# Performance work log

Hardware: AMD Instinct MI355X
Metric: run time of the kernel (lower is better)

## Reference

```python
import jax, jax.numpy as jnp
import numpy as np


def setup_inputs() -> dict:
    key = jax.random.key(0)
    ks = jax.random.split(key, 8)
    b, s1, s2 = 16, 512, 40
    video_dim, text_dim, attn_dim = 1024, 300, 256
    return {
        "video": jax.random.normal(ks[0], (b, s1, video_dim), dtype=jnp.float32),
        "text": jax.random.normal(ks[1], (b, s2, text_dim), dtype=jnp.float32),
        "w1": jax.random.normal(ks[2], (video_dim, attn_dim), dtype=jnp.float32),
        "w2": jax.random.normal(ks[3], (text_dim, attn_dim), dtype=jnp.float32),
        "w3": jax.random.normal(ks[4], (attn_dim, 1), dtype=jnp.float32),
        "bias": jax.random.normal(ks[5], (attn_dim,), dtype=jnp.float32),
        "w4": jax.random.normal(ks[6], (4 * attn_dim, 500), dtype=jnp.float32),
        "b4": jax.random.normal(ks[7], (500,), dtype=jnp.float32),
    }


def reference(video, text, w1, w2, w3, bias, w4, b4):
    # video: (b, s1, d1), text: (b, s2, d2)
    e = jnp.einsum("bsd,da->bsa", video, w1)   # (b, s1, a) -- also 'hh' in original
    f = jnp.einsum("btd,da->bta", text, w2)    # (b, s2, a)
    # additive attention energies: tanh over (b, s1, s2, a) broadcast sum
    h = jnp.tanh(e[:, :, None, :] + f[:, None, :, :] + bias)  # (b, s1, s2, a)
    logits = jnp.squeeze(jnp.einsum("bsta,ao->bsto", h, w3), -1)  # (b, s1, s2)
    # original expands logits over attn_dim then softmaxes dim=2; identical to
    # softmax over s2 of the scalar scores, broadcast afterwards.
    attn = jax.nn.softmax(logits, axis=2)  # (b, s1, s2)
    text_attn = jnp.einsum("bst,bta->bsa", attn, f)  # (b, s1, a)
    cont = jnp.concatenate(
        [e, text_attn, e * text_attn, e - text_attn], axis=-1
    )  # (b, s1, 4a)
    return jnp.tanh(cont) @ w4 + b4  # (b, s1, 500)
```

## Files before the change

kernel.cpp:

```cpp
#include <hip/hip_runtime.h>
#include <hip/hip_bf16.h>
#include <cstdint>

typedef __attribute__((ext_vector_type(8))) short bf16x8;
typedef __attribute__((ext_vector_type(4))) short bf16x4;
typedef __attribute__((ext_vector_type(4))) float f32x4;

#define TANH_SCALE 2.8853900817779268f
#define TANH_UNSCALE 0.34657359027997264f

__device__ __forceinline__ short cvt_bf16(float f) {
  union { float f; uint32_t u; } x; x.f = f;
  uint32_t r = x.u + 0x7FFFu + ((x.u >> 16) & 1u);
  return (short)(r >> 16);
}
__device__ __forceinline__ float bf16_to_f(short s) {
  union { uint32_t u; float f; } x; x.u = ((uint32_t)(uint16_t)s) << 16;
  return x.f;
}

__device__ __forceinline__ float tanh_fast(float x) {
  float e = __builtin_amdgcn_exp2f(x * TANH_SCALE);
  return 1.0f - 2.0f * __builtin_amdgcn_rcpf(e + 1.0f);
}
__device__ __forceinline__ float sig_pre(float xs) {
  float e = __builtin_amdgcn_exp2f(xs);
  return __builtin_amdgcn_rcpf(e + 1.0f);
}

__device__ __forceinline__ void split8(float4 a, float4 b, bf16x8& h, bf16x8& l) {
  float fa[8] = {a.x, a.y, a.z, a.w, b.x, b.y, b.z, b.w};
  uint32_t uh[8], ul[8];
  #pragma unroll
  for (int j = 0; j < 8; j++) {
    union { float f; uint32_t u; } x; x.f = fa[j];
    uh[j] = x.u;
    union { uint32_t u; float f; } t; t.u = x.u & 0xffff0000u;
    union { float f; uint32_t u; } y; y.f = fa[j] - t.f;
    ul[j] = y.u;
  }
  union { uint32_t w[4]; bf16x8 v; } H, L;
  #pragma unroll
  for (int j = 0; j < 4; j++) {
    H.w[j] = __builtin_amdgcn_perm(uh[2 * j + 1], uh[2 * j], 0x07060302u);
    L.w[j] = __builtin_amdgcn_perm(ul[2 * j + 1], ul[2 * j], 0x07060302u);
  }
  h = H.v; l = L.v;
}

__global__ __launch_bounds__(256) void k_prep(const float* __restrict__ text,
                                              const float* __restrict__ w1,
                                              const float* __restrict__ w2,
                                              const float* __restrict__ w4,
                                              short* __restrict__ w1h,
                                              short* __restrict__ w1l,
                                              short* __restrict__ w4T,
                                              short* __restrict__ th,
                                              short* __restrict__ tl,
                                              short* __restrict__ w2h,
                                              short* __restrict__ w2l) {
  __shared__ float tile[32][33];
  int bid = blockIdx.x;
  if (bid < 256) {
    int idx = bid;
    int r0 = (idx & 31) * 32, c0 = (idx >> 5) * 32;
    int j = threadIdx.x & 31, i0 = threadIdx.x >> 5;
    #pragma unroll
    for (int i = i0; i < 32; i += 8) tile[i][j] = w1[(size_t)(r0 + i) * 256 + c0 + j];
    __syncthreads();
    #pragma unroll
    for (int i = i0; i < 32; i += 8) {
      float v = tile[j][i];
      short h = cvt_bf16(v);
      w1h[(size_t)(c0 + i) * 1024 + r0 + j] = h;
      w1l[(size_t)(c0 + i) * 1024 + r0 + j] = cvt_bf16(v - bf16_to_f(h));
    }
  } else if (bid < 768) {
    int idx = bid - 256;
    int r0 = (idx & 31) * 32, c0 = (idx >> 5) * 32;
    int j = threadIdx.x & 31, i0 = threadIdx.x >> 5;
    #pragma unroll
    for (int i = i0; i < 32; i += 8) {
      int c = c0 + j;
      tile[i][j] = (c < 500) ? w4[(size_t)(r0 + i) * 500 + c] : 0.f;
    }
    __syncthreads();
    #pragma unroll
    for (int i = i0; i < 32; i += 8)
      w4T[(size_t)(c0 + i) * 1024 + r0 + j] = cvt_bf16(tile[j][i]);
  } else if (bid < 928) {
    int idx = bid - 768;
    int row = idx * 4 + (threadIdx.x >> 6);
    int cl = threadIdx.x & 63;
    const float* trow = text + (size_t)row * 300;
    short* hrow = th + (size_t)row * 320;
    short* lrow = tl + (size_t)row * 320;
    #pragma unroll
    for (int c0 = 0; c0 < 320; c0 += 64) {
      int c = c0 + cl;
      float v = (c < 300) ? trow[c] : 0.f;
      short h = cvt_bf16(v);
      hrow[c] = h;
      lrow[c] = cvt_bf16(v - bf16_to_f(h));
    }
  } else {
    int idx = bid - 928;
    int rt = idx % 10, ct = idx / 10;
    int r0 = rt * 32, c0 = ct * 32;
    int j = threadIdx.x & 31, i0 = threadIdx.x >> 5;
    #pragma unroll
    for (int i = i0; i < 32; i += 8) {
      int r = r0 + i;
      tile[i][j] = (r < 300) ? w2[(size_t)r * 256 + c0 + j] : 0.f;
    }
    __syncthreads();
    #pragma unroll
    for (int i = i0; i < 32; i += 8) {
      float v = tile[j][i];
      short h = cvt_bf16(v);
      w2h[(size_t)(c0 + i) * 320 + r0 + j] = h;
      w2l[(size_t)(c0 + i) * 320 + r0 + j] = cvt_bf16(v - bf16_to_f(h));
    }
  }
}

__device__ __forceinline__ void load_lds16(void* lds, const void* g) {
  __builtin_amdgcn_global_load_lds(
      (const __attribute__((address_space(1))) void*)g,
      (__attribute__((address_space(3))) void*)lds, 16, 0, 0);
}

__global__ __launch_bounds__(256) void k_gemm_big(const float* __restrict__ video,
                                                  const short* __restrict__ w1h,
                                                  const short* __restrict__ w1l,
                                                  const short* __restrict__ th,
                                                  const short* __restrict__ tl,
                                                  const short* __restrict__ w2h,
                                                  const short* __restrict__ w2l,
                                                  float* __restrict__ eparts,
                                                  float* __restrict__ fbuf) {
  __shared__ __align__(16) char smem[65536];
  int bid = blockIdx.x;
  int tid = threadIdx.x, lane = tid & 63, wave = tid >> 6;
  int mrow = lane & 15, quad = lane >> 4;

  if (bid < 512) {
    short (*Ash)[64] = (short (*)[64])(smem);
    short (*Asl)[64] = (short (*)[64])(smem + 16384);
    int m0 = (bid & 63) * 128, n0 = ((bid >> 6) & 3) * 64;
    int z = bid >> 8;
    int kz0 = z * 512;
    int wm = wave * 32;
    int lrow = lane >> 3, lseg = (lane & 7) * 8;

    f32x4 acc[2][4];
    #pragma unroll
    for (int i = 0; i < 2; i++)
      #pragma unroll
      for (int j = 0; j < 4; j++) acc[i][j] = (f32x4){0.f, 0.f, 0.f, 0.f};

    auto stageB = [&](int k0, int buf) {
      short* Bh = (short*)(smem + 32768 + buf * 8192);
      short* Bl = (short*)(smem + 49152 + buf * 8192);
      #pragma unroll
      for (int i = 0; i < 2; i++) {
        int c = wave * 2 + i;
        size_t go = (size_t)(n0 + c * 8 + lrow) * 1024 + k0 + lseg;
        load_lds16(Bh + (size_t)(c * 8) * 64, w1h + go);
        load_lds16(Bl + (size_t)(c * 8) * 64, w1l + go);
      }
    };
    auto loadA = [&](int k0, float4* va) {
      #pragma unroll
      for (int it = 0; it < 4; it++) {
        int idx = it * 256 + tid;
        const float* src = video + (size_t)(m0 + (idx >> 3)) * 1024 + k0 + (idx & 7) * 8;
        va[it * 2]     = *(const float4*)src;
        va[it * 2 + 1] = *(const float4*)(src + 4);
      }
    };

    float4 va[8];
    stageB(kz0, 0);
    loadA(kz0, va);

    for (int t = 0; t < 8; t++) {
      int k0 = kz0 + t * 64;
      int cur = t & 1;
      bf16x8 hi[4], lo[4];
      #pragma unroll
      for (int it = 0; it < 4; it++) split8(va[it * 2], va[it * 2 + 1], hi[it], lo[it]);
      __builtin_amdgcn_s_barrier();
      #pragma unroll
      for (int it = 0; it < 4; it++) {
        int idx = it * 256 + tid;
        *(bf16x8*)&Ash[idx >> 3][(idx & 7) * 8] = hi[it];
        *(bf16x8*)&Asl[idx >> 3][(idx & 7) * 8] = lo[it];
      }
      if (t + 1 < 8) {
        stageB(k0 + 64, cur ^ 1);
        loadA(k0 + 64, va);
        asm volatile("s_waitcnt vmcnt(12)" ::: "memory");
      } else {
        asm volatile("s_waitcnt vmcnt(0)" ::: "memory");
      }
      asm volatile("s_waitcnt lgkmcnt(0)" ::: "memory");
      __builtin_amdgcn_s_barrier();
      const short* Bh = (const short*)(smem + 32768 + cur * 8192);
      const short* Bl = (const short*)(smem + 49152 + cur * 8192);
      #pragma unroll
      for (int ks = 0; ks < 2; ks++) {
        int kk = ks * 32 + quad * 8;
        bf16x8 ah[2], al[2], bh[4], bl[4];
        #pragma unroll
        for (int i = 0; i < 2; i++) {
          ah[i] = *(const bf16x8*)&Ash[wm + i * 16 + mrow][kk];
          al[i] = *(const bf16x8*)&Asl[wm + i * 16 + mrow][kk];
        }
        #pragma unroll
        for (int j = 0; j < 4; j++) {
          bh[j] = *(const bf16x8*)&Bh[(size_t)(j * 16 + mrow) * 64 + kk];
          bl[j] = *(const bf16x8*)&Bl[(size_t)(j * 16 + mrow) * 64 + kk];
        }
        #pragma unroll
        for (int i = 0; i < 2; i++)
          #pragma unroll
          for (int j = 0; j < 4; j++) {
            acc[i][j] = __builtin_amdgcn_mfma_f32_16x16x32_bf16(ah[i], bh[j], acc[i][j], 0, 0, 0);
            acc[i][j] = __builtin_amdgcn_mfma_f32_16x16x32_bf16(ah[i], bl[j], acc[i][j], 0, 0, 0);
            acc[i][j] = __builtin_amdgcn_mfma_f32_16x16x32_bf16(al[i], bh[j], acc[i][j], 0, 0, 0);
          }
      }
    }
    float* C = eparts + (size_t)z * 8192 * 256;
    int rbase = quad * 4;
    #pragma unroll
    for (int i = 0; i < 2; i++)
      #pragma unroll
      for (int j = 0; j < 4; j++) {
        int col = n0 + j * 16 + mrow;
        #pragma unroll
        for (int r = 0; r < 4; r++) {
          int row = m0 + wm + i * 16 + rbase + r;
          C[(size_t)row * 256 + col] = acc[i][j][r];
        }
      }
  } else {
    short (*Ash)[72] = (short (*)[72])(smem);
    short (*Asl)[72] = (short (*)[72])(smem + 9216);
    short (*Bsh)[72] = (short (*)[72])(smem + 18432);
    short (*Bsl)[72] = (short (*)[72])(smem + 27648);
    int idx = bid - 512;
    int m0 = (idx % 10) * 64, n0 = (idx / 10) * 64;
    int wm = (wave & 1) * 32, wn = (wave >> 1) * 32;
    int srow = tid >> 3, sseg = (tid & 7) * 8;
    f32x4 acc[2][2];
    #pragma unroll
    for (int i = 0; i < 2; i++)
      #pragma unroll
      for (int j = 0; j < 2; j++) acc[i][j] = (f32x4){0.f, 0.f, 0.f, 0.f};

    for (int k0 = 0; k0 < 320; k0 += 64) {
      size_t aoff0 = (size_t)(m0 + srow) * 320 + k0 + sseg;
      size_t aoff1 = aoff0 + (size_t)32 * 320;
      size_t boff0 = (size_t)(n0 + srow) * 320 + k0 + sseg;
      size_t boff1 = boff0 + (size_t)32 * 320;
      bf16x8 a0h = *(const bf16x8*)(th + aoff0);
      bf16x8 a1h = *(const bf16x8*)(th + aoff1);
      bf16x8 a0l = *(const bf16x8*)(tl + aoff0);
      bf16x8 a1l = *(const bf16x8*)(tl + aoff1);
      bf16x8 b0h = *(const bf16x8*)(w2h + boff0);
      bf16x8 b1h = *(const bf16x8*)(w2h + boff1);
      bf16x8 b0l = *(const bf16x8*)(w2l + boff0);
      bf16x8 b1l = *(const bf16x8*)(w2l + boff1);
      __syncthreads();
      *(bf16x8*)&Ash[srow][sseg] = a0h;  *(bf16x8*)&Ash[srow + 32][sseg] = a1h;
      *(bf16x8*)&Asl[srow][sseg] = a0l;  *(bf16x8*)&Asl[srow + 32][sseg] = a1l;
      *(bf16x8*)&Bsh[srow][sseg] = b0h;  *(bf16x8*)&Bsh[srow + 32][sseg] = b1h;
      *(bf16x8*)&Bsl[srow][sseg] = b0l;  *(bf16x8*)&Bsl[srow + 32][sseg] = b1l;
      __syncthreads();
      #pragma unroll
      for (int ks = 0; ks < 2; ks++) {
        int kk = ks * 32 + quad * 8;
        bf16x8 ah[2], al[2], bh[2], bl[2];
        ah[0] = *(const bf16x8*)&Ash[wm + mrow][kk];
        ah[1] = *(const bf16x8*)&Ash[wm + 16 + mrow][kk];
        al[0] = *(const bf16x8*)&Asl[wm + mrow][kk];
        al[1] = *(const bf16x8*)&Asl[wm + 16 + mrow][kk];
        bh[0] = *(const bf16x8*)&Bsh[wn + mrow][kk];
        bh[1] = *(const bf16x8*)&Bsh[wn + 16 + mrow][kk];
        bl[0] = *(const bf16x8*)&Bsl[wn + mrow][kk];
        bl[1] = *(const bf16x8*)&Bsl[wn + 16 + mrow][kk];
        #pragma unroll
        for (int i = 0; i < 2; i++)
          #pragma unroll
          for (int j = 0; j < 2; j++) {
            acc[i][j] = __builtin_amdgcn_mfma_f32_16x16x32_bf16(ah[i], bh[j], acc[i][j], 0, 0, 0);
            acc[i][j] = __builtin_amdgcn_mfma_f32_16x16x32_bf16(ah[i], bl[j], acc[i][j], 0, 0, 0);
            acc[i][j] = __builtin_amdgcn_mfma_f32_16x16x32_bf16(al[i], bh[j], acc[i][j], 0, 0, 0);
          }
      }
    }
    int rbase = quad * 4;
    #pragma unroll
    for (int i = 0; i < 2; i++)
      #pragma unroll
      for (int j = 0; j < 2; j++) {
        int col = n0 + wn + j * 16 + mrow;
        #pragma unroll
        for (int r = 0; r < 4; r++) {
          int row = m0 + wm + i * 16 + rbase + r;
          fbuf[(size_t)row * 256 + col] = acc[i][j][r];
        }
      }
  }
}

__global__ __launch_bounds__(256) void k_gemm_f(const short* __restrict__ A,
                                                const short* __restrict__ BT,
                                                const float* __restrict__ bias,
                                                float* __restrict__ C,
                                                int K, int ldc, int nstore) {
  __shared__ __align__(16) short As[2][128][64];
  __shared__ __align__(16) short Bs[2][64][64];
  int m0 = blockIdx.x * 128, n0 = blockIdx.y * 64;
  int tid = threadIdx.x, lane = tid & 63, wave = tid >> 6;
  int wm = wave * 32;
  int mrow = lane & 15, quad = lane >> 4;
  int lrow = lane >> 3, lseg = (lane & 7) * 8;

  f32x4 acc[2][4];
  #pragma unroll
  for (int i = 0; i < 2; i++)
    #pragma unroll
    for (int j = 0; j < 4; j++) acc[i][j] = (f32x4){0.f, 0.f, 0.f, 0.f};

  auto stage = [&](int k0, int buf) {
    #pragma unroll
    for (int i = 0; i < 4; i++) {
      int c = wave * 4 + i;
      load_lds16(&As[buf][c * 8][0], A + (size_t)(m0 + c * 8 + lrow) * K + k0 + lseg);
    }
    #pragma unroll
    for (int i = 0; i < 2; i++) {
      int c = wave * 2 + i;
      load_lds16(&Bs[buf][c * 8][0], BT + (size_t)(n0 + c * 8 + lrow) * K + k0 + lseg);
    }
  };

  int NT = K >> 6;
  stage(0, 0);
  for (int t = 0; t < NT; t++) {
    int cur = t & 1;
    if (t + 1 < NT) {
      stage((t + 1) << 6, cur ^ 1);
      asm volatile("s_waitcnt vmcnt(6)" ::: "memory");
    } else {
      asm volatile("s_waitcnt vmcnt(0)" ::: "memory");
    }
    __builtin_amdgcn_s_barrier();
    #pragma unroll
    for (int ks = 0; ks < 2; ks++) {
      int kk = ks * 32 + quad * 8;
      bf16x8 af[2], bf[4];
      #pragma unroll
      for (int i = 0; i < 2; i++) af[i] = *(const bf16x8*)&As[cur][wm + i * 16 + mrow][kk];
      #pragma unroll
      for (int j = 0; j < 4; j++) bf[j] = *(const bf16x8*)&Bs[cur][j * 16 + mrow][kk];
      #pragma unroll
      for (int i = 0; i < 2; i++)
        #pragma unroll
        for (int j = 0; j < 4; j++)
          acc[i][j] = __builtin_amdgcn_mfma_f32_16x16x32_bf16(af[i], bf[j], acc[i][j], 0, 0, 0);
    }
    __builtin_amdgcn_s_barrier();
  }
  int rbase = quad * 4;
  #pragma unroll
  for (int i = 0; i < 2; i++)
    #pragma unroll
    for (int j = 0; j < 4; j++) {
      int col = n0 + j * 16 + mrow;
      if (col < nstore) {
        float bv = bias[col];
        #pragma unroll
        for (int r = 0; r < 4; r++) {
          int row = m0 + wm + i * 16 + rbase + r;
          C[(size_t)row * ldc + col] = acc[i][j][r] + bv;
        }
      }
    }
}

__global__ __launch_bounds__(512) void k_middle(const float* __restrict__ e0p,
                                                const float* __restrict__ e1p,
                                                const float* __restrict__ fb,
                                                const float* __restrict__ w3,
                                                const float* __restrict__ bias,
                                                short* __restrict__ cont) {
  __shared__ __align__(16) float fbs[40 * 256];
  __shared__ float lg[16][40];
  __shared__ float attn[16][40];
  int tid = threadIdx.x, wave = tid >> 6, lane = tid & 63;
  int la = lane & 31, half = lane >> 5;
  int row0 = blockIdx.x * 16;
  int b = row0 >> 9;
  int lgrow = wave + (half ? 8 : 0);
  int myrow = row0 + lgrow;

  const float4* fsrc = (const float4*)(fb + (size_t)b * 40 * 256);
  const float4* bias4 = (const float4*)bias;
  for (int i = tid; i < 40 * 64; i += 512) {
    float4 v = fsrc[i];
    float4 bb = bias4[i & 63];
    v.x = (v.x + bb.x) * TANH_SCALE; v.y = (v.y + bb.y) * TANH_SCALE;
    v.z = (v.z + bb.z) * TANH_SCALE; v.w = (v.w + bb.w) * TANH_SCALE;
    ((float4*)fbs)[i] = v;
  }
  __syncthreads();

  int a0 = la * 8;
  size_t eoff = (size_t)myrow * 256 + a0;
  float4 p00 = *(const float4*)(e0p + eoff);
  float4 p01 = *(const float4*)(e0p + eoff + 4);
  float4 p10 = *(const float4*)(e1p + eoff);
  float4 p11 = *(const float4*)(e1p + eoff + 4);
  float4 e0, e1;
  e0.x = p00.x + p10.x; e0.y = p00.y + p10.y; e0.z = p00.z + p10.z; e0.w = p00.w + p10.w;
  e1.x = p01.x + p11.x; e1.y = p01.y + p11.y; e1.z = p01.z + p11.z; e1.w = p01.w + p11.w;
  float4 w30 = *(const float4*)(w3 + a0);
  float4 w31 = *(const float4*)(w3 + a0 + 4);
  w30.x *= -2.f; w30.y *= -2.f; w30.z *= -2.f; w30.w *= -2.f;
  w31.x *= -2.f; w31.y *= -2.f; w31.z *= -2.f; w31.w *= -2.f;
  float4 bv0 = *(const float4*)(bias + a0);
  float4 bv1 = *(const float4*)(bias + a0 + 4);
  float4 es0, es1;
  es0.x = e0.x * TANH_SCALE; es0.y = e0.y * TANH_SCALE;
  es0.z = e0.z * TANH_SCALE; es0.w = e0.w * TANH_SCALE;
  es1.x = e1.x * TANH_SCALE; es1.y = e1.y * TANH_SCALE;
  es1.z = e1.z * TANH_SCALE; es1.w = e1.w * TANH_SCALE;

  for (int tc = 0; tc < 40; tc += 4) {
    float p[4];
    #pragma unroll
    for (int u = 0; u < 4; u++) {
      const float* fr = &fbs[(tc + u) * 256 + a0];
      float4 f0 = *(const float4*)fr;
      float4 f1 = *(const float4*)(fr + 4);
      p[u] = sig_pre(es0.x + f0.x) * w30.x + sig_pre(es0.y + f0.y) * w30.y
           + sig_pre(es0.z + f0.z) * w30.z + sig_pre(es0.w + f0.w) * w30.w
           + sig_pre(es1.x + f1.x) * w31.x + sig_pre(es1.y + f1.y) * w31.y
           + sig_pre(es1.z + f1.z) * w31.z + sig_pre(es1.w + f1.w) * w31.w;
    }
    #pragma unroll
    for (int s = 16; s >= 1; s >>= 1) {
      #pragma unroll
      for (int u = 0; u < 4; u++) p[u] += __shfl_xor(p[u], s, 64);
    }
    if (la == 0) {
      #pragma unroll
      for (int u = 0; u < 4; u++) lg[lgrow][tc + u] = p[u];
    }
  }

  auto softmax_row = [&](int r) {
    float x = (lane < 40) ? lg[r][lane] : -3.0e38f;
    float m = x;
    #pragma unroll
    for (int s = 32; s >= 1; s >>= 1) m = fmaxf(m, __shfl_xor(m, s, 64));
    float ex = (lane < 40) ? __builtin_amdgcn_exp2f((x - m) * 1.4426950408889634f) : 0.f;
    float ssum = ex;
    #pragma unroll
    for (int s = 32; s >= 1; s >>= 1) ssum += __shfl_xor(ssum, s, 64);
    if (lane < 40) attn[r][lane] = ex * __builtin_amdgcn_rcpf(ssum);
  };
  softmax_row(wave);
  softmax_row(wave + 8);

  float ac[8] = {0.f,0.f,0.f,0.f,0.f,0.f,0.f,0.f};
  for (int t = 0; t < 40; t++) {
    float w = attn[lgrow][t];
    const float* fr = &fbs[t * 256 + a0];
    float4 f0 = *(const float4*)fr;
    float4 f1 = *(const float4*)(fr + 4);
    ac[0] += w * f0.x; ac[1] += w * f0.y; ac[2] += w * f0.z; ac[3] += w * f0.w;
    ac[4] += w * f1.x; ac[5] += w * f1.y; ac[6] += w * f1.z; ac[7] += w * f1.w;
  }
  float tx[8];
  tx[0] = ac[0] * TANH_UNSCALE - bv0.x; tx[1] = ac[1] * TANH_UNSCALE - bv0.y;
  tx[2] = ac[2] * TANH_UNSCALE - bv0.z; tx[3] = ac[3] * TANH_UNSCALE - bv0.w;
  tx[4] = ac[4] * TANH_UNSCALE - bv1.x; tx[5] = ac[5] * TANH_UNSCALE - bv1.y;
  tx[6] = ac[6] * TANH_UNSCALE - bv1.z; tx[7] = ac[7] * TANH_UNSCALE - bv1.w;
  float ev[8] = {e0.x, e0.y, e0.z, e0.w, e1.x, e1.y, e1.z, e1.w};

  short* crow = cont + (size_t)myrow * 1024 + a0;
  auto st8 = [&](int off, const float* v) {
    bf16x8 pk;
    #pragma unroll
    for (int i = 0; i < 8; i++) pk[i] = cvt_bf16(v[i]);
    *(bf16x8*)(crow + off) = pk;
  };
  float s0[8], s1[8], s2[8], s3[8];
  #pragma unroll
  for (int i = 0; i < 8; i++) {
    s0[i] = tanh_fast(ev[i]);
    s1[i] = tanh_fast(tx[i]);
    s2[i] = tanh_fast(ev[i] * tx[i]);
    s3[i] = tanh_fast(ev[i] - tx[i]);
  }
  st8(0, s0); st8(256, s1); st8(512, s2); st8(768, s3);
}

extern "C" void kernel_launch(void* const* d_in, const int* in_sizes, int n_in,
                              void* d_out, int out_size, void* d_ws, size_t ws_size,
                              hipStream_t stream) {
  const float* video = (const float*)d_in[0];
  const float* text  = (const float*)d_in[1];
  const float* w1    = (const float*)d_in[2];
  const float* w2    = (const float*)d_in[3];
  const float* w3    = (const float*)d_in[4];
  const float* bias  = (const float*)d_in[5];
  const float* w4    = (const float*)d_in[6];
  const float* b4    = (const float*)d_in[7];
  float* out = (float*)d_out;
  char* ws = (char*)d_ws;

  short* contbuf  = (short*)(ws);
  short* w1T_hi   = (short*)(ws + 16777216);
  short* w1T_lo   = (short*)(ws + 17301504);
  short* w4T      = (short*)(ws + 17825792);
  float* fbuf     = (float*)(ws + 18874368);
  float* eparts   = (float*)(ws + 19529728);
  float* epart1   = (float*)(ws + 19529728 + 8388608);
  short* text_hi  = (short*)(ws + 36306944);
  short* text_lo  = (short*)(ws + 36716544);
  short* w2T_hi   = (short*)(ws + 37126144);
  short* w2T_lo   = (short*)(ws + 37330944);

  k_prep<<<1008, 256, 0, stream>>>(text, w1, w2, w4,
                                   w1T_hi, w1T_lo, w4T,
                                   text_hi, text_lo, w2T_hi, w2T_lo);
  k_gemm_big<<<552, 256, 0, stream>>>(video, w1T_hi, w1T_lo,
                                      text_hi, text_lo, w2T_hi, w2T_lo,
                                      eparts, fbuf);
  k_middle<<<512, 512, 0, stream>>>(eparts, epart1, fbuf, w3, bias, contbuf);
  k_gemm_f<<<dim3(64, 8), 256, 0, stream>>>(contbuf, w4T, b4, out, 1024, 500, 500);
}
```

Measured before the change: 163.7 us.

## Replace split-K video GEMM with 64x64 tiles and single-buffered full-K loop

The video×w1 GEMM previously used 128x64 tiles with split-K across two partial buffers, double-buffered B staging and explicit waitcnt pipelining; k_middle then summed the two partials. It now uses 64x64 tiles over the full K=1024 with a 2x2 wave layout and a single LDS buffer, writing e directly, so k_middle reads one buffer. This removes the partial-sum write/read traffic and halves the LDS footprint for better occupancy, but drops the async double-buffering overlap and lowers per-block reuse of the A tile.

```diff
diff --git a/kernel.cpp b/kernel.cpp
--- a/kernel.cpp
+++ b/kernel.cpp
@@ -137,42 +137,31 @@
                                                   const short* __restrict__ tl,
                                                   const short* __restrict__ w2h,
                                                   const short* __restrict__ w2l,
-                                                  float* __restrict__ eparts,
+                                                  float* __restrict__ ebuf,
                                                   float* __restrict__ fbuf) {
-  __shared__ __align__(16) char smem[65536];
+  __shared__ __align__(16) char smem[36864];
   int bid = blockIdx.x;
   int tid = threadIdx.x, lane = tid & 63, wave = tid >> 6;
   int mrow = lane & 15, quad = lane >> 4;
 
   if (bid < 512) {
     short (*Ash)[64] = (short (*)[64])(smem);
-    short (*Asl)[64] = (short (*)[64])(smem + 16384);
-    int m0 = (bid & 63) * 128, n0 = ((bid >> 6) & 3) * 64;
-    int z = bid >> 8;
-    int kz0 = z * 512;
-    int wm = wave * 32;
+    short (*Asl)[64] = (short (*)[64])(smem + 8192);
+    short (*Bsh)[64] = (short (*)[64])(smem + 16384);
+    short (*Bsl)[64] = (short (*)[64])(smem + 24576);
+    int m0 = (bid >> 2) * 64, n0 = (bid & 3) * 64;
+    int wm = (wave & 1) * 32, wn = (wave >> 1) * 32;
     int lrow = lane >> 3, lseg = (lane & 7) * 8;
 
-    f32x4 acc[2][4];
+    f32x4 acc[2][2];
     #pragma unroll
     for (int i = 0; i < 2; i++)
       #pragma unroll
-      for (int j = 0; j < 4; j++) acc[i][j] = (f32x4){0.f, 0.f, 0.f, 0.f};
-
-    auto stageB = [&](int k0, int buf) {
-      short* Bh = (short*)(smem + 32768 + buf * 8192);
-      short* Bl = (short*)(smem + 49152 + buf * 8192);
-      #pragma unroll
-      for (int i = 0; i < 2; i++) {
-        int c = wave * 2 + i;
-        size_t go = (size_t)(n0 + c * 8 + lrow) * 1024 + k0 + lseg;
-        load_lds16(Bh + (size_t)(c * 8) * 64, w1h + go);
-        load_lds16(Bl + (size_t)(c * 8) * 64, w1l + go);
-      }
-    };
+      for (int j = 0; j < 2; j++) acc[i][j] = (f32x4){0.f, 0.f, 0.f, 0.f};
+
     auto loadA = [&](int k0, float4* va) {
       #pragma unroll
-      for (int it = 0; it < 4; it++) {
+      for (int it = 0; it < 2; it++) {
         int idx = it * 256 + tid;
         const float* src = video + (size_t)(m0 + (idx >> 3)) * 1024 + k0 + (idx & 7) * 8;
         va[it * 2]     = *(const float4*)src;
@@ -180,69 +169,64 @@
       }
     };
 
-    float4 va[8];
-    stageB(kz0, 0);
-    loadA(kz0, va);
-
-    for (int t = 0; t < 8; t++) {
-      int k0 = kz0 + t * 64;
-      int cur = t & 1;
-      bf16x8 hi[4], lo[4];
-      #pragma unroll
-      for (int it = 0; it < 4; it++) split8(va[it * 2], va[it * 2 + 1], hi[it], lo[it]);
-      __builtin_amdgcn_s_barrier();
-      #pragma unroll
-      for (int it = 0; it < 4; it++) {
+    float4 va[4];
+    loadA(0, va);
+
+    for (int t = 0; t < 16; t++) {
+      int k0 = t * 64;
+      bf16x8 hi[2], lo[2];
+      #pragma unroll
+      for (int it = 0; it < 2; it++) split8(va[it * 2], va[it * 2 + 1], hi[it], lo[it]);
+      __syncthreads();
+      #pragma unroll
+      for (int it = 0; it < 2; it++) {
         int idx = it * 256 + tid;
         *(bf16x8*)&Ash[idx >> 3][(idx & 7) * 8] = hi[it];
         *(bf16x8*)&Asl[idx >> 3][(idx & 7) * 8] = lo[it];
       }
-      if (t + 1 < 8) {
-        stageB(k0 + 64, cur ^ 1);
-        loadA(k0 + 64, va);
-        asm volatile("s_waitcnt vmcnt(12)" ::: "memory");
-      } else {
-        asm volatile("s_waitcnt vmcnt(0)" ::: "memory");
-      }
-      asm volatile("s_waitcnt lgkmcnt(0)" ::: "memory");
-      __builtin_amdgcn_s_barrier();
-      const short* Bh = (const short*)(smem + 32768 + cur * 8192);
-      const short* Bl = (const short*)(smem + 49152 + cur * 8192);
+      #pragma unroll
+      for (int i = 0; i < 2; i++) {
+        int c = wave * 2 + i;
+        size_t go = (size_t)(n0 + c * 8 + lrow) * 1024 + k0 + lseg;
+        load_lds16(&Bsh[c * 8][0], w1h + go);
+        load_lds16(&Bsl[c * 8][0], w1l + go);
+      }
+      if (t + 1 < 16) loadA(k0 + 64, va);
+      __syncthreads();
       #pragma unroll
       for (int ks = 0; ks < 2; ks++) {
         int kk = ks * 32 + quad * 8;
-        bf16x8 ah[2], al[2], bh[4], bl[4];
+        bf16x8 ah[2], al[2], bh[2], bl[2];
         #pragma unroll
         for (int i = 0; i < 2; i++) {
           ah[i] = *(const bf16x8*)&Ash[wm + i * 16 + mrow][kk];
           al[i] = *(const bf16x8*)&Asl[wm + i * 16 + mrow][kk];
         }
         #pragma unroll
-        for (int j = 0; j < 4; j++) {
-          bh[j] = *(const bf16x8*)&Bh[(size_t)(j * 16 + mrow) * 64 + kk];
-          bl[j] = *(const bf16x8*)&Bl[(size_t)(j * 16 + mrow) * 64 + kk];
+        for (int j = 0; j < 2; j++) {
+          bh[j] = *(const bf16x8*)&Bsh[wn + j * 16 + mrow][kk];
+          bl[j] = *(const bf16x8*)&Bsl[wn + j * 16 + mrow][kk];
         }
         #pragma unroll
         for (int i = 0; i < 2; i++)
           #pragma unroll
-          for (int j = 0; j < 4; j++) {
+          for (int j = 0; j < 2; j++) {
             acc[i][j] = __builtin_amdgcn_mfma_f32_16x16x32_bf16(ah[i], bh[j], acc[i][j], 0, 0, 0);
             acc[i][j] = __builtin_amdgcn_mfma_f32_16x16x32_bf16(ah[i], bl[j], acc[i][j], 0, 0, 0);
             acc[i][j] = __builtin_amdgcn_mfma_f32_16x16x32_bf16(al[i], bh[j], acc[i][j], 0, 0, 0);
           }
       }
     }
-    float* C = eparts + (size_t)z * 8192 * 256;
     int rbase = quad * 4;
     #pragma unroll
     for (int i = 0; i < 2; i++)
       #pragma unroll
-      for (int j = 0; j < 4; j++) {
-        int col = n0 + j * 16 + mrow;
+      for (int j = 0; j < 2; j++) {
+        int col = n0 + wn + j * 16 + mrow;
         #pragma unroll
         for (int r = 0; r < 4; r++) {
           int row = m0 + wm + i * 16 + rbase + r;
-          C[(size_t)row * 256 + col] = acc[i][j][r];
+          ebuf[(size_t)row * 256 + col] = acc[i][j][r];
         }
       }
   } else {
@@ -392,8 +376,7 @@
     }
 }
 
-__global__ __launch_bounds__(512) void k_middle(const float* __restrict__ e0p,
-                                                const float* __restrict__ e1p,
+__global__ __launch_bounds__(512) void k_middle(const float* __restrict__ eb,
                                                 const float* __restrict__ fb,
                                                 const float* __restrict__ w3,
                                                 const float* __restrict__ bias,
@@ -421,13 +404,8 @@
 
   int a0 = la * 8;
   size_t eoff = (size_t)myrow * 256 + a0;
-  float4 p00 = *(const float4*)(e0p + eoff);
-  float4 p01 = *(const float4*)(e0p + eoff + 4);
-  float4 p10 = *(const float4*)(e1p + eoff);
-  float4 p11 = *(const float4*)(e1p + eoff + 4);
-  float4 e0, e1;
-  e0.x = p00.x + p10.x; e0.y = p00.y + p10.y; e0.z = p00.z + p10.z; e0.w = p00.w + p10.w;
-  e1.x = p01.x + p11.x; e1.y = p01.y + p11.y; e1.z = p01.z + p11.z; e1.w = p01.w + p11.w;
+  float4 e0 = *(const float4*)(eb + eoff);
+  float4 e1 = *(const float4*)(eb + eoff + 4);
   float4 w30 = *(const float4*)(w3 + a0);
   float4 w31 = *(const float4*)(w3 + a0 + 4);
   w30.x *= -2.f; w30.y *= -2.f; w30.z *= -2.f; w30.w *= -2.f;
@@ -530,8 +508,7 @@
   short* w1T_lo   = (short*)(ws + 17301504);
   short* w4T      = (short*)(ws + 17825792);
   float* fbuf     = (float*)(ws + 18874368);
-  float* eparts   = (float*)(ws + 19529728);
-  float* epart1   = (float*)(ws + 19529728 + 8388608);
+  float* ebuf     = (float*)(ws + 19529728);
   short* text_hi  = (short*)(ws + 36306944);
   short* text_lo  = (short*)(ws + 36716544);
   short* w2T_hi   = (short*)(ws + 37126144);
@@ -542,7 +519,7 @@
                                    text_hi, text_lo, w2T_hi, w2T_lo);
   k_gemm_big<<<552, 256, 0, stream>>>(video, w1T_hi, w1T_lo,
                                       text_hi, text_lo, w2T_hi, w2T_lo,
-                                      eparts, fbuf);
-  k_middle<<<512, 512, 0, stream>>>(eparts, epart1, fbuf, w3, bias, contbuf);
+                                      ebuf, fbuf);
+  k_middle<<<512, 512, 0, stream>>>(ebuf, fbuf, w3, bias, contbuf);
   k_gemm_f<<<dim3(64, 8), 256, 0, stream>>>(contbuf, w4T, b4, out, 1024, 500, 500);
 }
```

New measurement: 183.9 us. +12.3%, slower.
